# Kernel optimization log

Measured on AMD Instinct MI355X. Metric: run time of the kernel, lower is better.

## Reference

```python
import jax, jax.numpy as jnp
import numpy as np

B, N, BR, BC = 1024, 9, 3, 3
L = N * N                 # 81 cells
D, H, F = 512, 8, 2048
E = D // H                # 64 head dim
EPS = 1e-5


def _layernorm(x, g, b):
    m = jnp.mean(x, axis=-1, keepdims=True)
    v = jnp.mean(jnp.square(x - m), axis=-1, keepdims=True)
    return (x - m) * jax.lax.rsqrt(v + EPS) * g + b


def setup_inputs() -> dict:
    key = jax.random.key(0)
    ks = jax.random.split(key, 14)
    s = 0.02
    return {
        "src":   jax.random.normal(ks[0], (B, L, D), jnp.float32),
        # linear weights stored as (in, out) so y = x @ W + b (same math as torch x @ W.T + b)
        "w_qkv": jax.random.normal(ks[1], (D, 3 * D), jnp.float32) * s,
        "b_qkv": jnp.zeros((3 * D,), jnp.float32),
        "w_out": jax.random.normal(ks[2], (D, D), jnp.float32) * s,
        "b_out": jnp.zeros((D,), jnp.float32),
        "g1": jnp.ones((D,), jnp.float32),
        "beta1": jnp.zeros((D,), jnp.float32),
        "g2": jnp.ones((D,), jnp.float32),
        "beta2": jnp.zeros((D,), jnp.float32),
        "w_ff1": jax.random.normal(ks[3], (D, F), jnp.float32) * s,
        "b_ff1": jnp.zeros((F,), jnp.float32),
        "w_ff2": jax.random.normal(ks[4], (F, D), jnp.float32) * s,
        "b_ff2": jnp.zeros((D,), jnp.float32),
    }


def reference(src, w_qkv, b_qkv, w_out, b_out, g1, beta1, g2, beta2,
              w_ff1, b_ff1, w_ff2, b_ff2):
    # pre-norm attention
    x = _layernorm(src, g1, beta1)
    qkv = x @ w_qkv + b_qkv                       # (B, L, 3D)
    q, k, v = jnp.split(qkv, 3, axis=-1)
    rs = lambda t: t.reshape(B, N, N, H, E)       # (B, row, col, H, E)
    q2, k2, v2 = rs(q), rs(k), rs(v)
    scale = 1.0 / np.sqrt(E).astype(np.float32)

    # row attention: attend over columns within each row
    s_r = jnp.einsum('brqhe,brkhe->brhqk', q2, k2) * scale
    y_r = jnp.einsum('brhqk,brkhe->brqhe', jax.nn.softmax(s_r, axis=-1), v2)

    # column attention: attend over rows within each column
    s_c = jnp.einsum('bqche,bkche->bchqk', q2, k2) * scale
    y_c = jnp.einsum('bchqk,bkche->bqche', jax.nn.softmax(s_c, axis=-1), v2)

    # block attention: attend within each 3x3 block (9 cells)
    n_br, n_bc = N // BR, N // BC
    blk = lambda t: (t.reshape(B, n_br, BR, n_bc, BC, H, E)
                      .transpose(0, 1, 3, 2, 4, 5, 6)
                      .reshape(B, n_br, n_bc, BR * BC, H, E))
    qb, kb, vb = blk(q2), blk(k2), blk(v2)
    s_b = jnp.einsum('bijqhe,bijkhe->bijhqk', qb, kb) * scale
    y_b = jnp.einsum('bijhqk,bijkhe->bijqhe', jax.nn.softmax(s_b, axis=-1), vb)
    y_b = (y_b.reshape(B, n_br, n_bc, BR, BC, H, E)
              .transpose(0, 1, 3, 2, 4, 5, 6)
              .reshape(B, N, N, H, E))

    y = (y_r + y_c + y_b) / 3.0
    y = y.reshape(B, L, D) @ w_out + b_out

    x = src + y                                   # dropout = 0 (eval)
    residual = x
    h = _layernorm(x, g2, beta2)
    h = jax.nn.gelu(h @ w_ff1 + b_ff1, approximate=False) @ w_ff2 + b_ff2
    return residual + h
```

## Files before the change

kernel.cpp:

```cpp
#include <hip/hip_runtime.h>

#define BB 1024
#define NN 9
#define LL 81
#define DD 512
#define HH 8
#define EE 64
#define FF 2048
#define MM (BB*LL)
#define N3 (3*DD)

typedef unsigned short u16;
typedef __bf16 bf16x8 __attribute__((ext_vector_type(8)));
typedef float f32x4 __attribute__((ext_vector_type(4)));
typedef unsigned short u16x8 __attribute__((ext_vector_type(8)));

__device__ __forceinline__ float bf2f(u16 u) {
    return __uint_as_float(((unsigned int)u) << 16);
}
__device__ __forceinline__ u16 f2bf(float f) {
    unsigned int u = __float_as_uint(f);
    unsigned int r = u + 0x7fffu + ((u >> 16) & 1u);
    return (u16)(r >> 16);
}
__device__ __forceinline__ float gelu_fast(float x) {
    float u = 0.7978845608f * x * fmaf(0.044715f * x, x, 1.0f);
    float e = __expf(2.0f * u);
    float t = 1.0f - 2.0f / (e + 1.0f);
    return 0.5f * x * (1.0f + t);
}

#define GL16(g, l) __builtin_amdgcn_global_load_lds( \
    (const __attribute__((address_space(1))) void*)(g), \
    (__attribute__((address_space(3))) void*)(l), 16, 0, 0)

#define SB0 __builtin_amdgcn_sched_barrier(0)

__global__ __launch_bounds__(256) void prep_k(
    const float* __restrict__ src, const float* __restrict__ g1,
    const float* __restrict__ beta1, u16* __restrict__ xln,
    const float* __restrict__ w_qkv, u16* __restrict__ wqkvt,
    const float* __restrict__ w_out, u16* __restrict__ woutt,
    const float* __restrict__ w_ff1, u16* __restrict__ wff1t,
    const float* __restrict__ w_ff2, u16* __restrict__ wff2t) {
    const int tid = threadIdx.x;
    int ib = blockIdx.x;
    if (ib < MM / 4) {
        int row = ib * 4 + (tid >> 6);
        int lane = tid & 63;
        const float4* xp = (const float4*)(src + (long)row * DD);
        float4 a = xp[lane * 2], b = xp[lane * 2 + 1];
        float s  = a.x + a.y + a.z + a.w + b.x + b.y + b.z + b.w;
        float sq = a.x*a.x + a.y*a.y + a.z*a.z + a.w*a.w
                 + b.x*b.x + b.y*b.y + b.z*b.z + b.w*b.w;
#pragma unroll
        for (int off = 1; off < 64; off <<= 1) {
            s  += __shfl_xor(s, off);
            sq += __shfl_xor(sq, off);
        }
        float mean = s * (1.0f / 512.0f);
        float var  = sq * (1.0f / 512.0f) - mean * mean;
        float rstd = rsqrtf(var + 1e-5f);
        const float4* gp = (const float4*)(g1 + lane * 8);
        const float4* bp = (const float4*)(beta1 + lane * 8);
        float4 g0 = gp[0], g1v = gp[1], b0 = bp[0], b1v = bp[1];
        float xv[8] = {a.x,a.y,a.z,a.w,b.x,b.y,b.z,b.w};
        float gv[8] = {g0.x,g0.y,g0.z,g0.w,g1v.x,g1v.y,g1v.z,g1v.w};
        float bv[8] = {b0.x,b0.y,b0.z,b0.w,b1v.x,b1v.y,b1v.z,b1v.w};
        u16x8 ov;
#pragma unroll
        for (int j = 0; j < 8; ++j)
            ov[j] = f2bf((xv[j] - mean) * rstd * gv[j] + bv[j]);
        *(u16x8*)(xln + (long)row * DD + lane * 8) = ov;
        return;
    }
    ib -= MM / 4;
    const float* W; u16* Wt; int K, N;
    if (ib < 768)        { W = w_qkv; Wt = wqkvt; K = DD; N = N3; }
    else if (ib < 1024)  { ib -= 768;  W = w_out; Wt = woutt; K = DD; N = DD; }
    else if (ib < 2048)  { ib -= 1024; W = w_ff1; Wt = wff1t; K = DD; N = FF; }
    else                 { ib -= 2048; W = w_ff2; Wt = wff2t; K = FF; N = DD; }
    __shared__ float t[32][33];
    const int nbx = N / 32;
    const int n0 = (ib % nbx) * 32, k0 = (ib / nbx) * 32;
    const int tx = tid & 31, ty = tid >> 5;
#pragma unroll
    for (int i = 0; i < 32; i += 8)
        t[ty + i][tx] = W[(long)(k0 + ty + i) * N + n0 + tx];
    __syncthreads();
#pragma unroll
    for (int i = 0; i < 32; i += 8)
        Wt[(long)(n0 + ty + i) * K + k0 + tx] = f2bf(t[tx][ty + i]);
}

__global__ __launch_bounds__(256) void layernorm_b(const u16* __restrict__ X,
                                                   const float* __restrict__ g,
                                                   const float* __restrict__ be,
                                                   u16* __restrict__ Y) {
    int row = blockIdx.x * 4 + (threadIdx.x >> 6);
    int lane = threadIdx.x & 63;
    u16x8 xr = *(const u16x8*)(X + (long)row * DD + lane * 8);
    float xv[8];
#pragma unroll
    for (int j = 0; j < 8; ++j) xv[j] = bf2f(xr[j]);
    float s = 0.0f, sq = 0.0f;
#pragma unroll
    for (int j = 0; j < 8; ++j) { s += xv[j]; sq += xv[j] * xv[j]; }
#pragma unroll
    for (int off = 1; off < 64; off <<= 1) {
        s  += __shfl_xor(s, off);
        sq += __shfl_xor(sq, off);
    }
    float mean = s * (1.0f / 512.0f);
    float var  = sq * (1.0f / 512.0f) - mean * mean;
    float rstd = rsqrtf(var + 1e-5f);
    const float4* gp = (const float4*)(g + lane * 8);
    const float4* bp = (const float4*)(be + lane * 8);
    float4 g0 = gp[0], g1v = gp[1], b0 = bp[0], b1v = bp[1];
    float gv[8] = {g0.x,g0.y,g0.z,g0.w,g1v.x,g1v.y,g1v.z,g1v.w};
    float bv[8] = {b0.x,b0.y,b0.z,b0.w,b1v.x,b1v.y,b1v.z,b1v.w};
    u16x8 ov;
#pragma unroll
    for (int j = 0; j < 8; ++j)
        ov[j] = f2bf((xv[j] - mean) * rstd * gv[j] + bv[j]);
    *(u16x8*)(Y + (long)row * DD + lane * 8) = ov;
}

enum { EPI_BF16_BIAS = 0, EPI_BF16_RESID = 1, EPI_BF16_GELU = 2, EPI_F32_XADD = 3 };

template <int EPI>
__global__ __launch_bounds__(256, 2) void gemm_bt(
    const u16* __restrict__ A, int lda,
    const u16* __restrict__ Bt, int ldb,
    const float* __restrict__ bias,
    const float* __restrict__ residF,
    const u16* __restrict__ residB,
    u16* __restrict__ outB, float* __restrict__ outF,
    int N, int K, int nbn) {
    __shared__ u16 smem[36864];
    u16* const Asb = smem;
    u16* const Bsb = smem + 24576;
    const int tid = threadIdx.x;
    const int lane = tid & 63;
    const int w = tid >> 6;
    const int wr = w >> 1, wc = w & 1;

    const int cpx = gridDim.x >> 3;
    const int bid = (blockIdx.x & 7) * cpx + (blockIdx.x >> 3);
    const int bm = bid / nbn, bn = bid % nbn;
    const long Arow0 = (long)bm * 256;
    const long Brow0 = (long)bn * 128;

    auto stage = [&](int buf, int kt) {
        const u16* abase = A + Arow0 * (long)lda + (long)kt * 32;
        const u16* bbase = Bt + Brow0 * (long)ldb + (long)kt * 32;
#pragma unroll
        for (int u = 0; u < 4; ++u) {
            const int c = tid + u * 256;
            const int row = c >> 2;
            const int col = ((c & 3) ^ ((row >> 1) & 3)) * 8;
            GL16(abase + (long)row * lda + col, Asb + buf * 8192 + c * 8);
        }
#pragma unroll
        for (int u = 0; u < 2; ++u) {
            const int c = tid + u * 256;
            const int row = c >> 2;
            const int col = ((c & 3) ^ ((row >> 1) & 3)) * 8;
            GL16(bbase + (long)row * ldb + col, Bsb + buf * 4096 + c * 8);
        }
    };

    f32x4 acc[8][4] = {};
    const int fr = lane & 15;
    const int s8 = lane >> 4;
    const int sl = (s8 ^ ((fr >> 1) & 3)) * 8;

    const int nk = K / 32;
    stage(0, 0); stage(1, 1);

    int cur = 0;
    for (int kt = 0; kt < nk; ++kt) {
        if (kt + 1 < nk) { asm volatile("s_waitcnt vmcnt(6)" ::: "memory"); }
        else             { asm volatile("s_waitcnt vmcnt(0)" ::: "memory"); }
        SB0;
        __builtin_amdgcn_s_barrier();
        SB0;

        bf16x8 af[8], bb[4];
        const u16* Ab = Asb + cur * 8192;
        const u16* Bb = Bsb + cur * 4096;
#pragma unroll
        for (int mt = 0; mt < 8; ++mt)
            af[mt] = *(const bf16x8*)(Ab + (wr * 128 + mt * 16 + fr) * 32 + sl);
#pragma unroll
        for (int nt = 0; nt < 4; ++nt)
            bb[nt] = *(const bf16x8*)(Bb + (wc * 64 + nt * 16 + fr) * 32 + sl);

        if (kt + 2 < nk) {
            int nb = cur + 2; if (nb >= 3) nb -= 3;
            stage(nb, kt + 2);
        }

        asm volatile("s_waitcnt lgkmcnt(0)" ::: "memory");
        SB0;
#pragma unroll
        for (int mt = 0; mt < 8; ++mt)
#pragma unroll
            for (int nt = 0; nt < 4; ++nt)
                acc[mt][nt] = __builtin_amdgcn_mfma_f32_16x16x32_bf16(af[mt], bb[nt], acc[mt][nt], 0, 0, 0);
        cur = cur + 1; if (cur == 3) cur = 0;
    }

    if (EPI == EPI_BF16_BIAS || EPI == EPI_BF16_GELU || EPI == EPI_BF16_RESID) {
        __builtin_amdgcn_s_barrier();
        u16 (*eps)[132] = (u16(*)[132])smem;
#pragma unroll
        for (int nt = 0; nt < 4; ++nt) {
            const int cl = wc * 64 + nt * 16 + fr;
            const float bv = bias ? bias[bn * 128 + cl] : 0.0f;
#pragma unroll
            for (int mt = 0; mt < 8; ++mt) {
                const int rl = wr * 128 + mt * 16 + s8 * 4;
#pragma unroll
                for (int q = 0; q < 4; ++q) {
                    float v = acc[mt][nt][q] + bv;
                    if (EPI == EPI_BF16_GELU) v = gelu_fast(v);
                    if (EPI == EPI_BF16_RESID)
                        v += residF[(Arow0 + rl + q) * (long)N + bn * 128 + cl];
                    eps[rl + q][cl] = f2bf(v);
                }
            }
        }
        __syncthreads();
#pragma unroll
        for (int u = 0; u < 16; ++u) {
            const int i = u * 256 + tid;
            const int row = i >> 4, cc = (i & 15) * 8;
            u16x8 vv = *(const u16x8*)&eps[row][cc];
            *(u16x8*)(outB + (Arow0 + row) * (long)N + bn * 128 + cc) = vv;
        }
    } else {
        float (*epf)[132] = (float(*)[132])smem;
#pragma unroll
        for (int h = 0; h < 2; ++h) {
            __syncthreads();
            if (wr == h) {
#pragma unroll
                for (int nt = 0; nt < 4; ++nt) {
                    const int cl = wc * 64 + nt * 16 + fr;
                    const float bv = bias ? bias[bn * 128 + cl] : 0.0f;
#pragma unroll
                    for (int mt = 0; mt < 8; ++mt) {
                        const int rl = mt * 16 + s8 * 4;
#pragma unroll
                        for (int q = 0; q < 4; ++q)
                            epf[rl + q][cl] = acc[mt][nt][q] + bv;
                    }
                }
            }
            __syncthreads();
#pragma unroll
            for (int u = 0; u < 16; ++u) {
                const int i = u * 256 + tid;
                const int row = i >> 5, cc = (i & 31) * 4;
                const long gr = (Arow0 + h * 128 + row) * (long)N + bn * 128 + cc;
                float4 vv = *(const float4*)&epf[row][cc];
                ushort4 rb = *(const ushort4*)(residB + gr);
                vv.x += bf2f(rb.x); vv.y += bf2f(rb.y);
                vv.z += bf2f(rb.z); vv.w += bf2f(rb.w);
                *(float4*)(outF + gr) = vv;
            }
        }
    }
}

__global__ __launch_bounds__(256) void attn_k(u16* __restrict__ qkv) {
    __shared__ u16 S[96][104];
    __shared__ u16 Wm[96][104];
    __shared__ u16 Vt[64][104];
    const int bh = blockIdx.x;
    const int b = bh >> 3, h = bh & 7;
    u16* qbase = qkv + (long)b * LL * N3 + h * EE;
    const u16* kbase = qbase + DD;
    const u16* vbase = qbase + 2 * DD;
    const int tid = threadIdx.x;
    const int lane = tid & 63;
    const int w = tid >> 6;
    const int fr = lane & 15, s8 = lane >> 4;

    {
        u16x8 z = {};
        u16* wp = &Wm[0][0];
        for (int i = tid; i < (96 * 104) / 8; i += 256)
            *(u16x8*)(wp + i * 8) = z;
        for (int i = tid; i < 64 * 16; i += 256) {
            int e = i >> 4, c = i & 15;
            if (c < 15) Vt[e][81 + c] = 0;
        }
        for (int i = tid; i < 81 * 16; i += 256) {
            int cell = i >> 4, e0 = (i & 15) * 4;
            ushort4 v = *(const ushort4*)(vbase + (long)cell * N3 + e0);
            Vt[e0][cell] = v.x; Vt[e0 + 1][cell] = v.y;
            Vt[e0 + 2][cell] = v.z; Vt[e0 + 3][cell] = v.w;
        }
    }

    for (int i = 0; i < 9; ++i) {
        const int tile = w + 4 * i;
        const int qt = tile / 6, kt = tile % 6;
        int qc = qt * 16 + fr; if (qc > 80) qc = 80;
        int kc = kt * 16 + fr; if (kc > 80) kc = 80;
        const u16* qp = qbase + (long)qc * N3 + s8 * 8;
        const u16* kp = kbase + (long)kc * N3 + s8 * 8;
        bf16x8 a0 = *(const bf16x8*)qp;
        bf16x8 a1 = *(const bf16x8*)(qp + 32);
        bf16x8 b0 = *(const bf16x8*)kp;
        bf16x8 b1 = *(const bf16x8*)(kp + 32);
        f32x4 acc = {};
        acc = __builtin_amdgcn_mfma_f32_16x16x32_bf16(a0, b0, acc, 0, 0, 0);
        acc = __builtin_amdgcn_mfma_f32_16x16x32_bf16(a1, b1, acc, 0, 0, 0);
#pragma unroll
        for (int q = 0; q < 4; ++q)
            S[qt * 16 + s8 * 4 + q][kt * 16 + fr] = f2bf(acc[q]);
    }
    __syncthreads();

    if (tid < 81) {
        const int q = tid;
        const int r = q / 9, c = q % 9;
#pragma unroll
        for (int t = 0; t < 3; ++t) {
            int mm[9];
            if (t == 0) {
#pragma unroll
                for (int j = 0; j < 9; ++j) mm[j] = r * 9 + j;
            } else if (t == 1) {
#pragma unroll
                for (int j = 0; j < 9; ++j) mm[j] = j * 9 + c;
            } else {
                const int br = (r / 3) * 3, bc = (c / 3) * 3;
#pragma unroll
                for (int j = 0; j < 9; ++j) mm[j] = (br + j / 3) * 9 + bc + j % 3;
            }
            float sc[9], mx = -1e30f;
#pragma unroll
            for (int j = 0; j < 9; ++j) {
                sc[j] = bf2f(S[q][mm[j]]) * 0.125f;
                mx = fmaxf(mx, sc[j]);
            }
            float sum = 0.0f;
#pragma unroll
            for (int j = 0; j < 9; ++j) { sc[j] = __expf(sc[j] - mx); sum += sc[j]; }
            const float inv = 1.0f / (3.0f * sum);
#pragma unroll
            for (int j = 0; j < 9; ++j) {
                u16* p = &Wm[q][mm[j]];
                *p = f2bf(bf2f(*p) + sc[j] * inv);
            }
        }
    }
    __syncthreads();

    for (int i = 0; i < 6; ++i) {
        const int tile = w + 4 * i;
        const int qt = tile % 6, et = tile / 6;
        f32x4 acc = {};
#pragma unroll
        for (int kc = 0; kc < 3; ++kc) {
            bf16x8 a  = *(const bf16x8*)&Vt[et * 16 + fr][kc * 32 + s8 * 8];
            bf16x8 bf = *(const bf16x8*)&Wm[qt * 16 + fr][kc * 32 + s8 * 8];
            acc = __builtin_amdgcn_mfma_f32_16x16x32_bf16(a, bf, acc, 0, 0, 0);
        }
        const int q = qt * 16 + fr;
        if (q < 81) {
            ushort4 o;
            o.x = f2bf(acc[0]); o.y = f2bf(acc[1]);
            o.z = f2bf(acc[2]); o.w = f2bf(acc[3]);
            *(ushort4*)(qbase + (long)q * N3 + et * 16 + s8 * 4) = o;
        }
    }
}

extern "C" void kernel_launch(void* const* d_in, const int* in_sizes, int n_in,
                              void* d_out, int out_size, void* d_ws, size_t ws_size,
                              hipStream_t stream) {
    const float* src    = (const float*)d_in[0];
    const float* w_qkv  = (const float*)d_in[1];
    const float* b_qkv  = (const float*)d_in[2];
    const float* w_out  = (const float*)d_in[3];
    const float* b_out  = (const float*)d_in[4];
    const float* g1     = (const float*)d_in[5];
    const float* beta1  = (const float*)d_in[6];
    const float* g2     = (const float*)d_in[7];
    const float* beta2  = (const float*)d_in[8];
    const float* w_ff1  = (const float*)d_in[9];
    const float* b_ff1  = (const float*)d_in[10];
    const float* w_ff2  = (const float*)d_in[11];
    const float* b_ff2  = (const float*)d_in[12];
    float* out = (float*)d_out;

    char* ws = (char*)d_ws;
    u16* wqkvt = (u16*)(ws + 0);
    u16* woutt = (u16*)(ws + 1572864);
    u16* wff1t = (u16*)(ws + 2097152);
    u16* wff2t = (u16*)(ws + 4194304);
    u16* bufA  = (u16*)(ws + 6291456);
    u16* bufB  = (u16*)(ws + 6291456 + 84934656ULL);
    u16* hln   = bufB;
    u16* h1    = bufB + (size_t)MM * DD;

    const int nbm  = MM / 256;
    const int nbmh = (MM / 2) / 256;

    prep_k<<<MM / 4 + 3072, 256, 0, stream>>>(
        src, g1, beta1, bufA,
        w_qkv, wqkvt, w_out, woutt, w_ff1, wff1t, w_ff2, wff2t);

    gemm_bt<EPI_BF16_BIAS><<<nbm * (N3 / 128), 256, 0, stream>>>(
        bufA, DD, wqkvt, DD, b_qkv, nullptr, nullptr, bufB, nullptr, N3, DD, N3 / 128);

    attn_k<<<BB * HH, 256, 0, stream>>>(bufB);

    gemm_bt<EPI_BF16_RESID><<<nbm * (DD / 128), 256, 0, stream>>>(
        bufB, N3, woutt, DD, b_out, src, nullptr, bufA, nullptr, DD, DD, DD / 128);

    layernorm_b<<<MM / 4, 256, 0, stream>>>(bufA, g2, beta2, hln);

    for (int mh = 0; mh < 2; ++mh) {
        const size_t roff = (size_t)mh * (MM / 2);
        gemm_bt<EPI_BF16_GELU><<<nbmh * (FF / 128), 256, 0, stream>>>(
            hln + roff * DD, DD, wff1t, DD, b_ff1, nullptr, nullptr,
            h1, nullptr, FF, DD, FF / 128);
        gemm_bt<EPI_F32_XADD><<<nbmh * (DD / 128), 256, 0, stream>>>(
            h1, FF, wff2t, FF, b_ff2, nullptr, bufA + roff * DD,
            nullptr, out + roff * DD, DD, FF, DD / 128);
    }
}
```

Measured before the change: 1.063 ms.

## Split FFN along hidden dim instead of rows, accumulating FF2 partials in fp32 output

The FFN is now chunked along the hidden dimension F (two 1024-wide halves) over all rows, rather than splitting rows into two halves. The first FF2 pass writes fp32 partial sums to the output, and the second reads them back and adds the bias and the residual. Each GEMM launch gets a larger grid, and the intermediate buffer stays the same size. In exchange the fp32 output makes an extra round trip through memory and the FF2 K dimension is halved per launch.

```diff
diff --git a/kernel.cpp b/kernel.cpp
--- a/kernel.cpp
+++ b/kernel.cpp
@@ -126,7 +126,8 @@
     *(u16x8*)(Y + (long)row * DD + lane * 8) = ov;
 }
 
-enum { EPI_BF16_BIAS = 0, EPI_BF16_RESID = 1, EPI_BF16_GELU = 2, EPI_F32_XADD = 3 };
+enum { EPI_BF16_BIAS = 0, EPI_BF16_RESID = 1, EPI_BF16_GELU = 2,
+       EPI_F32_PART = 3, EPI_F32_FINAL = 4 };
 
 template <int EPI>
 __global__ __launch_bounds__(256, 2) void gemm_bt(
@@ -265,9 +266,12 @@
                 const int row = i >> 5, cc = (i & 31) * 4;
                 const long gr = (Arow0 + h * 128 + row) * (long)N + bn * 128 + cc;
                 float4 vv = *(const float4*)&epf[row][cc];
-                ushort4 rb = *(const ushort4*)(residB + gr);
-                vv.x += bf2f(rb.x); vv.y += bf2f(rb.y);
-                vv.z += bf2f(rb.z); vv.w += bf2f(rb.w);
+                if (EPI == EPI_F32_FINAL) {
+                    float4 pp = *(const float4*)(outF + gr);
+                    ushort4 rb = *(const ushort4*)(residB + gr);
+                    vv.x += pp.x + bf2f(rb.x); vv.y += pp.y + bf2f(rb.y);
+                    vv.z += pp.z + bf2f(rb.z); vv.w += pp.w + bf2f(rb.w);
+                }
                 *(float4*)(outF + gr) = vv;
             }
         }
@@ -407,10 +411,9 @@
     u16* bufA  = (u16*)(ws + 6291456);
     u16* bufB  = (u16*)(ws + 6291456 + 84934656ULL);
     u16* hln   = bufB;
-    u16* h1    = bufB + (size_t)MM * DD;
-
-    const int nbm  = MM / 256;
-    const int nbmh = (MM / 2) / 256;
+    u16* h1c   = bufB + (size_t)MM * DD;
+
+    const int nbm = MM / 256;
 
     prep_k<<<MM / 4 + 3072, 256, 0, stream>>>(
         src, g1, beta1, bufA,
@@ -426,13 +429,17 @@
 
     layernorm_b<<<MM / 4, 256, 0, stream>>>(bufA, g2, beta2, hln);
 
-    for (int mh = 0; mh < 2; ++mh) {
-        const size_t roff = (size_t)mh * (MM / 2);
-        gemm_bt<EPI_BF16_GELU><<<nbmh * (FF / 128), 256, 0, stream>>>(
-            hln + roff * DD, DD, wff1t, DD, b_ff1, nullptr, nullptr,
-            h1, nullptr, FF, DD, FF / 128);
-        gemm_bt<EPI_F32_XADD><<<nbmh * (DD / 128), 256, 0, stream>>>(
-            h1, FF, wff2t, FF, b_ff2, nullptr, bufA + roff * DD,
-            nullptr, out + roff * DD, DD, FF, DD / 128);
-    }
-}
+    for (int c = 0; c < 2; ++c) {
+        gemm_bt<EPI_BF16_GELU><<<nbm * (1024 / 128), 256, 0, stream>>>(
+            hln, DD, wff1t + (size_t)c * 1024 * DD, DD, b_ff1 + c * 1024, nullptr,
+            nullptr, h1c, nullptr, 1024, DD, 1024 / 128);
+        if (c == 0)
+            gemm_bt<EPI_F32_PART><<<nbm * (DD / 128), 256, 0, stream>>>(
+                h1c, 1024, wff2t, FF, nullptr, nullptr, nullptr,
+                nullptr, out, DD, 1024, DD / 128);
+        else
+            gemm_bt<EPI_F32_FINAL><<<nbm * (DD / 128), 256, 0, stream>>>(
+                h1c, 1024, wff2t + 1024, FF, b_ff2, nullptr, bufA,
+                nullptr, out, DD, 1024, DD / 128);
+    }
+}
```

Measured after the change: 1.134 ms. 6.7% more time.
